# Kernel tuning notes

Hardware: AMD Instinct MI355X
Metric: run time of the kernel (lower is better)

Reference implementation:

```python
import jax, jax.numpy as jnp
import numpy as np
from jax import lax

D_MODEL = 1024
D_INNER = 2048   # expand * d_model
D_STATE = 16
DT_RANK = 64     # ceil(d_model / 16)
D_CONV = 4
B, L = 2, 1024


def setup_inputs() -> dict:
    key = jax.random.key(0)
    ks = jax.random.split(key, 8)
    s = 0.02
    x = jax.random.normal(ks[0], (B, L, D_MODEL), dtype=jnp.float32)
    in_proj_w = jax.random.normal(ks[1], (2 * D_INNER, D_MODEL), dtype=jnp.float32) * s
    conv_w = jax.random.normal(ks[2], (D_INNER, D_CONV), dtype=jnp.float32) * s  # depthwise kernel
    conv_b = jax.random.normal(ks[3], (D_INNER,), dtype=jnp.float32) * s
    x_proj_w = jax.random.normal(ks[4], (DT_RANK + 2 * D_STATE, D_INNER), dtype=jnp.float32) * s
    dt_proj_w = jax.random.normal(ks[5], (D_INNER, DT_RANK), dtype=jnp.float32) * s
    dt_proj_b = jax.random.normal(ks[6], (D_INNER,), dtype=jnp.float32) * s
    A_log = jnp.log(jnp.broadcast_to(jnp.arange(1, D_STATE + 1, dtype=jnp.float32), (D_INNER, D_STATE)))
    D = jnp.ones((D_INNER,), dtype=jnp.float32)
    out_proj_w = jax.random.normal(ks[7], (D_MODEL, D_INNER), dtype=jnp.float32) * s
    return {"x": x, "in_proj_w": in_proj_w, "conv_w": conv_w, "conv_b": conv_b,
            "x_proj_w": x_proj_w, "dt_proj_w": dt_proj_w, "dt_proj_b": dt_proj_b,
            "A_log": A_log, "D": D, "out_proj_w": out_proj_w}


def _causal_depthwise_conv(x, conv_w, conv_b):
    # x: (B, L, d_inner); torch Conv1d(padding=d_conv-1) then [:, :, :L] == causal left pad
    Lx = x.shape[1]
    k = conv_w.shape[-1]
    xp = jnp.pad(x, ((0, 0), (k - 1, 0), (0, 0)))
    out = conv_b
    # small fixed kernel width (4): unrolled taps, fully vectorized over B,L,D
    out = sum(xp[:, i:i + Lx, :] * conv_w[:, i] for i in range(k)) + conv_b
    return out


def mamba_forward(x, in_proj_w, conv_w, conv_b, x_proj_w, dt_proj_w, dt_proj_b, A_log, D, out_proj_w):
    xz = x @ in_proj_w.T                       # (B, L, 2*d_inner)
    xi, z = xz[..., :D_INNER], xz[..., D_INNER:]
    xc = jax.nn.silu(_causal_depthwise_conv(xi, conv_w, conv_b))  # (B, L, d_inner)

    x_dbl = xc @ x_proj_w.T                    # (B, L, dt_rank + 2*d_state)
    dt = x_dbl[..., :DT_RANK]
    Bm = x_dbl[..., DT_RANK:DT_RANK + D_STATE]  # (B, L, N)
    Cm = x_dbl[..., DT_RANK + D_STATE:]         # (B, L, N)
    delta = jax.nn.softplus(dt @ dt_proj_w.T + dt_proj_b)  # (B, L, d_inner)

    A = -jnp.exp(A_log)                        # (d_inner, N)
    deltaA = jnp.exp(delta[..., None] * A)                           # (B, L, D, N)
    deltaBx = delta[..., None] * Bm[:, :, None, :] * xc[..., None]   # (B, L, D, N)

    def step(h, inp):
        dA, dBx, Ct = inp                      # (B,D,N), (B,D,N), (B,N)
        h = dA * h + dBx
        y = jnp.einsum('bdn,bn->bd', h, Ct)
        return h, y

    h0 = jnp.zeros((x.shape[0], D_INNER, D_STATE), dtype=x.dtype)
    _, ys = lax.scan(step, h0, (deltaA.transpose(1, 0, 2, 3),
                                deltaBx.transpose(1, 0, 2, 3),
                                Cm.transpose(1, 0, 2)))
    y = ys.transpose(1, 0, 2)                  # (B, L, d_inner)
    y = y + xc * D
    y = y * jax.nn.silu(z)
    return y @ out_proj_w.T                    # (B, L, d_model)


def reference(x, in_proj_w, conv_w, conv_b, x_proj_w, dt_proj_w, dt_proj_b, A_log, D, out_proj_w):
    return mamba_forward(x, in_proj_w, conv_w, conv_b, x_proj_w, dt_proj_w, dt_proj_b, A_log, D, out_proj_w)
```

## Files before the change

kernel.cpp:

```cpp
#include <hip/hip_runtime.h>
#include <hip/hip_bf16.h>
#include <cstdint>
#include <cstddef>

#define DMODEL 1024
#define DINNER 2048
#define NSTATE 16
#define DTRANK 64
#define BATCH 2
#define SEQ 1024
#define ROWS (BATCH*SEQ)
#define NCHUNK 16
#define CLEN (SEQ/NCHUNK)
#define KSPLIT 16

typedef __attribute__((ext_vector_type(8))) short short8;
typedef __attribute__((ext_vector_type(4))) float f32x4;

__device__ __forceinline__ float bf2f(__hip_bfloat16 h){ return __bfloat162float(h); }
__device__ __forceinline__ float sigmoidf_(float x){ return 1.0f/(1.0f + __expf(-x)); }

__device__ __forceinline__ void gld16(const void* g, void* l){
  __builtin_amdgcn_global_load_lds((const __attribute__((address_space(1))) void*)g,
                                   (__attribute__((address_space(3))) void*)l, 16, 0, 0);
}

__global__ void sniff_k(const unsigned short* __restrict__ xu, int* __restrict__ flag)
{
  int t = threadIdx.x;
  int cnt = 0;
  for (int i = t; i < 1024; i += 64) {
    unsigned short u = xu[i];
    int e = (u >> 7) & 0xFF;
    if (e >= 0x70 && e <= 0x86) cnt++;
  }
  for (int o = 32; o; o >>= 1) cnt += __shfl_down(cnt, o);
  if (t == 0) *flag = (cnt >= 768) ? 0 : 1;
}

struct CvtArgs {
  const void *s0,*s1,*s2,*s3,*s4,*s5,*s6,*s7,*s8,*s9;
  __hip_bfloat16 *xB,*inpB,*xprojB,*dtprojB,*outpB;
  float *cwF,*cbF,*dtbF,*alF,*DF;
  float *outZ;
  const int* flag;
};
#define CVT_C1 2097152
#define CVT_C2 6291456
#define CVT_C3 6299648
#define CVT_C4 6301696
#define CVT_C5 6498304
#define CVT_C6 6629376
#define CVT_C7 6631424
#define CVT_C8 6664192
#define CVT_C9 6666240
#define CVT_TOT 8763392

__device__ __forceinline__ float cvt_read(const void* s, int j, int fl){
  return fl ? ((const float*)s)[j] : bf2f(((const __hip_bfloat16*)s)[j]);
}

__global__ __launch_bounds__(256)
void convert_all_k(CvtArgs a)
{
  int i = blockIdx.x * 256 + threadIdx.x;
  const int fl = *a.flag;

  if (blockIdx.x < 2048) {
    f32x4 z = {0.f, 0.f, 0.f, 0.f};
    ((f32x4*)a.outZ)[i] = z;
  }

  if (i >= CVT_TOT) return;
  if (i < CVT_C1)      a.xB[i]                = __float2bfloat16(cvt_read(a.s0, i, fl));
  else if (i < CVT_C2) a.inpB[i-CVT_C1]       = __float2bfloat16(cvt_read(a.s1, i-CVT_C1, fl));
  else if (i < CVT_C3) a.cwF[i-CVT_C2]        = cvt_read(a.s2, i-CVT_C2, fl);
  else if (i < CVT_C4) a.cbF[i-CVT_C3]        = cvt_read(a.s3, i-CVT_C3, fl);
  else if (i < CVT_C5) a.xprojB[i-CVT_C4]     = __float2bfloat16(cvt_read(a.s4, i-CVT_C4, fl));
  else if (i < CVT_C6) a.dtprojB[i-CVT_C5]    = __float2bfloat16(cvt_read(a.s5, i-CVT_C5, fl));
  else if (i < CVT_C7) a.dtbF[i-CVT_C6]       = cvt_read(a.s6, i-CVT_C6, fl);
  else if (i < CVT_C8) a.alF[i-CVT_C7]        = cvt_read(a.s7, i-CVT_C7, fl);
  else if (i < CVT_C9) a.DF[i-CVT_C8]         = cvt_read(a.s8, i-CVT_C8, fl);
  else                 a.outpB[i-CVT_C9]      = __float2bfloat16(cvt_read(a.s9, i-CVT_C9, fl));
}

template<int EPI>
__global__ __launch_bounds__(256)
void gemm64(const __hip_bfloat16* __restrict__ A,
            const __hip_bfloat16* __restrict__ W,
            int M, int N, int K, int kchunk,
            float* __restrict__ outF,
            __hip_bfloat16* __restrict__ outH,
            const float* __restrict__ biasF)
{
  __shared__ alignas(16) __hip_bfloat16 As[128*64];
  __shared__ alignas(16) __hip_bfloat16 Ws[128*64];
  const int tid  = threadIdx.x;
  const int lane = tid & 63;
  const int wave = tid >> 6;
  const int wm = wave & 1, wn = wave >> 1;
  const int row0 = blockIdx.y * 128;
  const int col0 = blockIdx.x * 128;

  f32x4 acc[4][4] = {};

  int kbeg = 0, kend = K;
  if (EPI == 5 || EPI == 6) { kbeg = blockIdx.z * kchunk; kend = kbeg + kchunk; }

  const int r16 = lane & 15, q = lane >> 4;
  const int sx0 = ((q ^ (r16 & 7)) * 16);

  for (int k0 = kbeg; k0 < kend; k0 += 64) {
#pragma unroll
    for (int j = 0; j < 4; ++j) {
      int e = tid + j*256;
      int r = e >> 3, g = e & 7;
      int kc = ((g ^ (r & 7)) << 3);
      gld16(A + (size_t)(row0 + r) * K + k0 + kc, (char*)As + (size_t)e*16);
    }
#pragma unroll
    for (int j = 0; j < 4; ++j) {
      int e = tid + j*256;
      int r = e >> 3, g = e & 7;
      int kc = ((g ^ (r & 7)) << 3);
      int rw = col0 + r; if (EPI == 5 && rw > N-1) rw = N-1;
      gld16(W + (size_t)rw * K + k0 + kc, (char*)Ws + (size_t)e*16);
    }
    __syncthreads();

    const char* Ab = (const char*)As + ((wm*64 + r16) * 128);
    const char* Wb = (const char*)Ws + ((wn*64 + r16) * 128);
#pragma unroll
    for (int ksub = 0; ksub < 2; ++ksub) {
      const int sx = sx0 ^ (ksub * 64);
      short8 af[4], wf[4];
#pragma unroll
      for (int i = 0; i < 4; ++i) af[i] = *(const short8*)(Ab + i*16*128 + sx);
#pragma unroll
      for (int i = 0; i < 4; ++i) wf[i] = *(const short8*)(Wb + i*16*128 + sx);
#pragma unroll
      for (int mt = 0; mt < 4; ++mt)
#pragma unroll
        for (int nt = 0; nt < 4; ++nt)
          acc[mt][nt] = __builtin_amdgcn_mfma_f32_16x16x32_bf16(af[mt], wf[nt], acc[mt][nt], 0, 0, 0);
    }
    __syncthreads();
  }

  const int mbase = row0 + wm*64 + (q * 4);
  const int nbase = col0 + wn*64 + r16;

  float bv[4];
  if (EPI == 3) {
#pragma unroll
    for (int nt = 0; nt < 4; ++nt) bv[nt] = biasF[nbase + nt*16];
  }

#pragma unroll
  for (int mt = 0; mt < 4; ++mt) {
#pragma unroll
    for (int nt = 0; nt < 4; ++nt) {
#pragma unroll
      for (int r = 0; r < 4; ++r) {
        int row = mbase + mt*16 + r;
        int col = nbase + nt*16;
        float v = acc[mt][nt][r];
        if (EPI == 3) {
          v += bv[nt];
          float sp = fmaxf(v, 0.0f) + __logf(1.0f + __expf(-fabsf(v)));
          outF[(size_t)row * DINNER + col] = sp;
        } else if (EPI == 4) {
          if (col < DINNER) {
            outH[(size_t)row * DINNER + col] = __float2bfloat16(v);
          } else {
            outF[(size_t)row * DINNER + (col - DINNER)] = v * sigmoidf_(v);
          }
        } else if (EPI == 5) {
          if (col < 96)
            outF[(size_t)blockIdx.z * (ROWS*96) + (size_t)row * 96 + col] = v;
        } else if (EPI == 6) {
          unsafeAtomicAdd(&outF[(size_t)row * DMODEL + col], v);
        }
      }
    }
  }
}

__global__ __launch_bounds__(256)
void reduce_xdbl_k(const float* __restrict__ part, float* __restrict__ xdbl,
                   __hip_bfloat16* __restrict__ dtH)
{
  int i = blockIdx.x * 256 + threadIdx.x;
  if (i >= ROWS*96) return;
  float s = 0.f;
#pragma unroll
  for (int kc = 0; kc < KSPLIT; ++kc) s += part[(size_t)kc*ROWS*96 + i];
  xdbl[i] = s;
  int row = i / 96, col = i - row*96;
  if (col < 64) dtH[(size_t)row*64 + col] = __float2bfloat16(s);
}

__global__ __launch_bounds__(256)
void conv_silu_k(const __hip_bfloat16* __restrict__ xi,
                 const float* __restrict__ cw,
                 const float* __restrict__ cb,
                 __hip_bfloat16* __restrict__ xcH)
{
  int idx = blockIdx.x * 256 + threadIdx.x;
  if (idx >= ROWS * DINNER) return;
  int d  = idx & (DINNER - 1);
  int t  = (idx >> 11) & (SEQ - 1);
  int bt = idx >> 11;
  float acc = cb[d];
#pragma unroll
  for (int i = 0; i < 4; ++i) {
    int tt = t - 3 + i;
    if (tt >= 0) acc += cw[d*4 + i] * bf2f(xi[(size_t)(bt - 3 + i) * DINNER + d]);
  }
  float y = acc * sigmoidf_(acc);
  xcH[idx] = __float2bfloat16(y);
}

#define GSTEP 8

__global__ __launch_bounds__(256)
void stats_k(const float* __restrict__ delta,
             const __hip_bfloat16* __restrict__ xcH,
             const float* __restrict__ xdbl,
             const float* __restrict__ alF,
             float* __restrict__ Hc, float* __restrict__ Sd)
{
  __shared__ alignas(16) float Bs[CLEN*16];
  const int bid  = blockIdx.x;
  const int b    = bid >> 9;
  const int c    = (bid >> 5) & (NCHUNK-1);
  const int cg   = bid & 31;
  const int tid  = threadIdx.x;
  const int lane = tid & 63;
  const int wave = tid >> 6;
  const int sub  = lane & 3;
  const int ch   = (cg << 6) + (wave << 4) + (lane >> 2);

  const size_t rb = (size_t)b * SEQ + (size_t)c * CLEN;

  for (int i = tid; i < CLEN*16; i += 256) {
    int t = i >> 4, j = i & 15;
    Bs[i] = xdbl[(rb + t)*96 + 64 + j];
  }
  __syncthreads();

  float negA[4];
#pragma unroll
  for (int j = 0; j < 4; ++j) negA[j] = -__expf(alF[ch*NSTATE + sub*4 + j]);

  const float*          dp = delta + rb * DINNER + ch;
  const __hip_bfloat16* xp = xcH   + rb * DINNER + ch;

  float h0=0.f,h1=0.f,h2=0.f,h3=0.f, sd=0.f;
  float d0[GSTEP], x0[GSTEP], d1[GSTEP], x1[GSTEP];

#define PF1(D_,X_,T0) \
  _Pragma("unroll") \
  for (int u = 0; u < GSTEP; ++u) { \
    D_[u] = dp[(size_t)((T0)+u) * DINNER]; \
    X_[u] = bf2f(xp[(size_t)((T0)+u) * DINNER]); \
  }
#define ST1(D_,X_,T0) \
  _Pragma("unroll") \
  for (int u = 0; u < GSTEP; ++u) { \
    float d_ = D_[u]; \
    sd += d_; \
    float du = d_ * X_[u]; \
    f32x4 B4 = *(const f32x4*)&Bs[((T0)+u)*16 + sub*4]; \
    h0 = __expf(d_*negA[0])*h0 + du*B4.x; \
    h1 = __expf(d_*negA[1])*h1 + du*B4.y; \
    h2 = __expf(d_*negA[2])*h2 + du*B4.z; \
    h3 = __expf(d_*negA[3])*h3 + du*B4.w; \
  }

  PF1(d0, x0, 0)
  for (int t0 = 0; t0 < CLEN; t0 += 2*GSTEP) {
    PF1(d1, x1, t0 + GSTEP)
    ST1(d0, x0, t0)
    if (t0 + 2*GSTEP < CLEN) { PF1(d0, x0, t0 + 2*GSTEP) }
    ST1(d1, x1, t0 + GSTEP)
  }
#undef PF1
#undef ST1

  const size_t bc = (size_t)(b*NCHUNK + c);
  f32x4 hv = { h0, h1, h2, h3 };
  *(f32x4*)&Hc[(bc*DINNER + ch)*NSTATE + sub*4] = hv;
  if (sub == 0) Sd[bc*DINNER + ch] = sd;
}

__global__ __launch_bounds__(256)
void carry_k(const float* __restrict__ Hc, const float* __restrict__ Sd,
             const float* __restrict__ alF, float* __restrict__ hin)
{
  int i = blockIdx.x * 256 + threadIdx.x;
  int n  = i & (NSTATE-1);
  int ch = (i >> 4) & (DINNER-1);
  int b  = i >> 15;
  float negA = -__expf(alF[ch * NSTATE + n]);
  float h = 0.f;
#pragma unroll
  for (int c = 0; c < NCHUNK; ++c) {
    size_t bc = (size_t)(b*NCHUNK + c);
    hin[(bc*DINNER + ch)*NSTATE + n] = h;
    float P = __expf(negA * Sd[bc*DINNER + ch]);
    h = P * h + Hc[(bc*DINNER + ch)*NSTATE + n];
  }
}

__global__ __launch_bounds__(256)
void emit_k(const float* __restrict__ delta,
            const __hip_bfloat16* __restrict__ xcH,
            const float* __restrict__ xdbl,
            const float* __restrict__ zsF,
            const float* __restrict__ alF,
            const float* __restrict__ DF,
            const float* __restrict__ hin,
            __hip_bfloat16* __restrict__ yH)
{
  __shared__ alignas(16) float BCs[CLEN*32];
  const int bid  = blockIdx.x;
  const int b    = bid >> 9;
  const int c    = (bid >> 5) & (NCHUNK-1);
  const int cg   = bid & 31;
  const int tid  = threadIdx.x;
  const int lane = tid & 63;
  const int wave = tid >> 6;
  const int sub  = lane & 3;
  const int ch   = (cg << 6) + (wave << 4) + (lane >> 2);

  const size_t rb = (size_t)b * SEQ + (size_t)c * CLEN;

  for (int i = tid; i < CLEN*32; i += 256) {
    int t = i >> 5, j = i & 31;
    BCs[i] = xdbl[(rb + t)*96 + 64 + j];
  }
  __syncthreads();

  float negA[4];
#pragma unroll
  for (int j = 0; j < 4; ++j) negA[j] = -__expf(alF[ch*NSTATE + sub*4 + j]);
  const float Dch = DF[ch];

  const float*          dp = delta + rb * DINNER + ch;
  const __hip_bfloat16* xp = xcH   + rb * DINNER + ch;
  const float*          zp = zsF   + rb * DINNER + ch;
  __hip_bfloat16*       yp = yH    + rb * DINNER + ch;

  f32x4 hv = *(const f32x4*)&hin[((size_t)(b*NCHUNK + c)*DINNER + ch)*NSTATE + sub*4];
  float h0=hv.x, h1=hv.y, h2=hv.z, h3=hv.w;

  float d0[GSTEP], x0[GSTEP], z0[GSTEP], d1[GSTEP], x1[GSTEP], z1[GSTEP];

#define PF(D_,X_,Z_,T0) \
  _Pragma("unroll") \
  for (int u = 0; u < GSTEP; ++u) { \
    D_[u] = dp[(size_t)((T0)+u) * DINNER]; \
    X_[u] = bf2f(xp[(size_t)((T0)+u) * DINNER]); \
    Z_[u] = zp[(size_t)((T0)+u) * DINNER]; \
  }
#define STEPS(D_,X_,Z_,T0) \
  _Pragma("unroll") \
  for (int u = 0; u < GSTEP; ++u) { \
    float d_ = D_[u]; \
    float du = d_ * X_[u]; \
    f32x4 B4 = *(const f32x4*)&BCs[((T0)+u)*32 + sub*4]; \
    f32x4 C4 = *(const f32x4*)&BCs[((T0)+u)*32 + 16 + sub*4]; \
    h0 = __expf(d_*negA[0])*h0 + du*B4.x; \
    h1 = __expf(d_*negA[1])*h1 + du*B4.y; \
    h2 = __expf(d_*negA[2])*h2 + du*B4.z; \
    h3 = __expf(d_*negA[3])*h3 + du*B4.w; \
    float p = h0*C4.x + h1*C4.y + h2*C4.z + h3*C4.w; \
    p += __shfl_xor(p, 1); \
    p += __shfl_xor(p, 2); \
    if (sub == 0) { \
      float y = (p + X_[u] * Dch) * Z_[u]; \
      yp[(size_t)((T0)+u) * DINNER] = __float2bfloat16(y); \
    } \
  }

  PF(d0, x0, z0, 0)
  for (int t0 = 0; t0 < CLEN; t0 += 2*GSTEP) {
    PF(d1, x1, z1, t0 + GSTEP)
    STEPS(d0, x0, z0, t0)
    if (t0 + 2*GSTEP < CLEN) { PF(d0, x0, z0, t0 + 2*GSTEP) }
    STEPS(d1, x1, z1, t0 + GSTEP)
  }
#undef PF
#undef STEPS
}

extern "C" void kernel_launch(void* const* d_in, const int* in_sizes, int n_in,
                              void* d_out, int out_size, void* d_ws, size_t ws_size,
                              hipStream_t stream)
{
  float* out = (float*)d_out;
  char* ws = (char*)d_ws;
  const size_t MB = 1024*1024;

  int*            flag    = (int*)            (ws);
  float*          cwF     = (float*)          (ws + 1024);
  float*          cbF     = (float*)          (ws + 40*1024);
  float*          dtbF    = (float*)          (ws + 56*1024);
  float*          alF     = (float*)          (ws + 72*1024);
  float*          DF      = (float*)          (ws + 208*1024);
  float*          Sd      = (float*)          (ws + 256*1024);
  __hip_bfloat16* xB      = (__hip_bfloat16*) (ws + 1*MB);
  __hip_bfloat16* inpB    = (__hip_bfloat16*) (ws + 5*MB);
  __hip_bfloat16* xiB     = (__hip_bfloat16*) (ws + 13*MB);
  float*          part    = (float*)          (ws + 1*MB);
  float*          dlt     = (float*)          (ws + 1*MB);
  __hip_bfloat16* xprojB  = (__hip_bfloat16*) (ws + 21*MB);
  __hip_bfloat16* dtprojB = (__hip_bfloat16*) (ws + 21*MB + 512*1024);
  __hip_bfloat16* outpB   = (__hip_bfloat16*) (ws + 22*MB);
  float*          zsF     = (float*)          (ws + 26*MB);
  __hip_bfloat16* xcH     = (__hip_bfloat16*) (ws + 42*MB);
  float*          xdbl    = (float*)          (ws + 50*MB);
  __hip_bfloat16* dtH     = (__hip_bfloat16*) (ws + 51*MB);
  __hip_bfloat16* yH      = (__hip_bfloat16*) (ws + 52*MB);
  float*          Hc      = (float*)          (ws + 60*MB);
  float*          hin     = (float*)          (ws + 64*MB);

  dim3 blk(256);

  sniff_k<<<1, 64, 0, stream>>>((const unsigned short*)d_in[0], flag);
  CvtArgs ca = { d_in[0], d_in[1], d_in[2], d_in[3], d_in[4],
                 d_in[5], d_in[6], d_in[7], d_in[8], d_in[9],
                 xB, inpB, xprojB, dtprojB, outpB,
                 cwF, cbF, dtbF, alF, DF, out, flag };
  convert_all_k<<<CVT_TOT/256, blk, 0, stream>>>(ca);

  gemm64<4><<<dim3(4096/128, ROWS/128), blk, 0, stream>>>(
      xB, inpB, ROWS, 2*DINNER, DMODEL, 0, zsF, xiB, nullptr);

  conv_silu_k<<<(ROWS*DINNER)/256, blk, 0, stream>>>(xiB, cwF, cbF, xcH);

  gemm64<5><<<dim3(1, ROWS/128, KSPLIT), blk, 0, stream>>>(
      xcH, xprojB, ROWS, 96, DINNER, DINNER/KSPLIT, part, nullptr, nullptr);
  reduce_xdbl_k<<<(ROWS*96+255)/256, blk, 0, stream>>>(part, xdbl, dtH);

  gemm64<3><<<dim3(DINNER/128, ROWS/128), blk, 0, stream>>>(
      dtH, dtprojB, ROWS, DINNER, DTRANK, 0, dlt, nullptr, dtbF);

  stats_k<<<BATCH*NCHUNK*32, blk, 0, stream>>>(dlt, xcH, xdbl, alF, Hc, Sd);
  carry_k<<<(BATCH*DINNER*NSTATE)/256, blk, 0, stream>>>(Hc, Sd, alF, hin);
  emit_k<<<BATCH*NCHUNK*32, blk, 0, stream>>>(dlt, xcH, xdbl, zsF, alF, DF, hin, yH);

  gemm64<6><<<dim3(DMODEL/128, ROWS/128, 4), blk, 0, stream>>>(
      yH, outpB, ROWS, DMODEL, DINNER, DINNER/4, out, nullptr, nullptr);
}
```

Baseline: 264.2 us.

## Vectorize input conversion, store gate in bf16, deepen scan prefetch

```diff
diff --git a/kernel.cpp b/kernel.cpp
--- a/kernel.cpp
+++ b/kernel.cpp
@@ -15,10 +15,19 @@
 #define KSPLIT 16
 
 typedef __attribute__((ext_vector_type(8))) short short8;
+typedef __attribute__((ext_vector_type(4))) short short4v;
 typedef __attribute__((ext_vector_type(4))) float f32x4;
 
 __device__ __forceinline__ float bf2f(__hip_bfloat16 h){ return __bfloat162float(h); }
 __device__ __forceinline__ float sigmoidf_(float x){ return 1.0f/(1.0f + __expf(-x)); }
+__device__ __forceinline__ unsigned short f2bfbits(float v){
+  __hip_bfloat16 h = __float2bfloat16(v);
+  return *(unsigned short*)&h;
+}
+__device__ __forceinline__ float bfbits2f(unsigned short u){
+  unsigned int x = ((unsigned int)u) << 16;
+  return *(float*)&x;
+}
 
 __device__ __forceinline__ void gld16(const void* g, void* l){
   __builtin_amdgcn_global_load_lds((const __attribute__((address_space(1))) void*)g,
@@ -55,33 +64,53 @@
 #define CVT_C8 6664192
 #define CVT_C9 6666240
 #define CVT_TOT 8763392
-
-__device__ __forceinline__ float cvt_read(const void* s, int j, int fl){
-  return fl ? ((const float*)s)[j] : bf2f(((const __hip_bfloat16*)s)[j]);
+#define CVT_BLOCKS (CVT_TOT/4/256)
+
+__device__ __forceinline__ void cvt_read4(const void* s, int j, int fl, float v[4]){
+  if (fl) {
+    f32x4 t = ((const f32x4*)s)[j>>2];
+    v[0]=t.x; v[1]=t.y; v[2]=t.z; v[3]=t.w;
+  } else {
+    short4v t = *(const short4v*)((const __hip_bfloat16*)s + j);
+    v[0]=bfbits2f((unsigned short)t.x); v[1]=bfbits2f((unsigned short)t.y);
+    v[2]=bfbits2f((unsigned short)t.z); v[3]=bfbits2f((unsigned short)t.w);
+  }
+}
+__device__ __forceinline__ void cvt_wB(__hip_bfloat16* d, int j, const float v[4]){
+  short4v o;
+  o.x=(short)f2bfbits(v[0]); o.y=(short)f2bfbits(v[1]);
+  o.z=(short)f2bfbits(v[2]); o.w=(short)f2bfbits(v[3]);
+  *(short4v*)(d + j) = o;
+}
+__device__ __forceinline__ void cvt_wF(float* d, int j, const float v[4]){
+  f32x4 o = { v[0], v[1], v[2], v[3] };
+  *(f32x4*)(d + j) = o;
 }
 
 __global__ __launch_bounds__(256)
 void convert_all_k(CvtArgs a)
 {
-  int i = blockIdx.x * 256 + threadIdx.x;
+  int i4 = blockIdx.x * 256 + threadIdx.x;
   const int fl = *a.flag;
 
   if (blockIdx.x < 2048) {
     f32x4 z = {0.f, 0.f, 0.f, 0.f};
-    ((f32x4*)a.outZ)[i] = z;
-  }
-
+    ((f32x4*)a.outZ)[i4] = z;
+  }
+
+  int i = i4 * 4;
   if (i >= CVT_TOT) return;
-  if (i < CVT_C1)      a.xB[i]                = __float2bfloat16(cvt_read(a.s0, i, fl));
-  else if (i < CVT_C2) a.inpB[i-CVT_C1]       = __float2bfloat16(cvt_read(a.s1, i-CVT_C1, fl));
-  else if (i < CVT_C3) a.cwF[i-CVT_C2]        = cvt_read(a.s2, i-CVT_C2, fl);
-  else if (i < CVT_C4) a.cbF[i-CVT_C3]        = cvt_read(a.s3, i-CVT_C3, fl);
-  else if (i < CVT_C5) a.xprojB[i-CVT_C4]     = __float2bfloat16(cvt_read(a.s4, i-CVT_C4, fl));
-  else if (i < CVT_C6) a.dtprojB[i-CVT_C5]    = __float2bfloat16(cvt_read(a.s5, i-CVT_C5, fl));
-  else if (i < CVT_C7) a.dtbF[i-CVT_C6]       = cvt_read(a.s6, i-CVT_C6, fl);
-  else if (i < CVT_C8) a.alF[i-CVT_C7]        = cvt_read(a.s7, i-CVT_C7, fl);
-  else if (i < CVT_C9) a.DF[i-CVT_C8]         = cvt_read(a.s8, i-CVT_C8, fl);
-  else                 a.outpB[i-CVT_C9]      = __float2bfloat16(cvt_read(a.s9, i-CVT_C9, fl));
+  float v[4];
+  if (i < CVT_C1)      { cvt_read4(a.s0, i, fl, v);        cvt_wB(a.xB, i, v); }
+  else if (i < CVT_C2) { cvt_read4(a.s1, i-CVT_C1, fl, v); cvt_wB(a.inpB, i-CVT_C1, v); }
+  else if (i < CVT_C3) { cvt_read4(a.s2, i-CVT_C2, fl, v); cvt_wF(a.cwF, i-CVT_C2, v); }
+  else if (i < CVT_C4) { cvt_read4(a.s3, i-CVT_C3, fl, v); cvt_wF(a.cbF, i-CVT_C3, v); }
+  else if (i < CVT_C5) { cvt_read4(a.s4, i-CVT_C4, fl, v); cvt_wB(a.xprojB, i-CVT_C4, v); }
+  else if (i < CVT_C6) { cvt_read4(a.s5, i-CVT_C5, fl, v); cvt_wB(a.dtprojB, i-CVT_C5, v); }
+  else if (i < CVT_C7) { cvt_read4(a.s6, i-CVT_C6, fl, v); cvt_wF(a.dtbF, i-CVT_C6, v); }
+  else if (i < CVT_C8) { cvt_read4(a.s7, i-CVT_C7, fl, v); cvt_wF(a.alF, i-CVT_C7, v); }
+  else if (i < CVT_C9) { cvt_read4(a.s8, i-CVT_C8, fl, v); cvt_wF(a.DF, i-CVT_C8, v); }
+  else                 { cvt_read4(a.s9, i-CVT_C9, fl, v); cvt_wB(a.outpB, i-CVT_C9, v); }
 }
 
 template<int EPI>
@@ -91,6 +120,7 @@
             int M, int N, int K, int kchunk,
             float* __restrict__ outF,
             __hip_bfloat16* __restrict__ outH,
+            __hip_bfloat16* __restrict__ outH2,
             const float* __restrict__ biasF)
 {
   __shared__ alignas(16) __hip_bfloat16 As[128*64];
@@ -173,7 +203,7 @@
           if (col < DINNER) {
             outH[(size_t)row * DINNER + col] = __float2bfloat16(v);
           } else {
-            outF[(size_t)row * DINNER + (col - DINNER)] = v * sigmoidf_(v);
+            outH2[(size_t)row * DINNER + (col - DINNER)] = __float2bfloat16(v * sigmoidf_(v));
           }
         } else if (EPI == 5) {
           if (col < 96)
@@ -221,7 +251,7 @@
   xcH[idx] = __float2bfloat16(y);
 }
 
-#define GSTEP 8
+#define GSTEP 16
 
 __global__ __launch_bounds__(256)
 void stats_k(const float* __restrict__ delta,
@@ -317,7 +347,7 @@
 void emit_k(const float* __restrict__ delta,
             const __hip_bfloat16* __restrict__ xcH,
             const float* __restrict__ xdbl,
-            const float* __restrict__ zsF,
+            const __hip_bfloat16* __restrict__ zsH,
             const float* __restrict__ alF,
             const float* __restrict__ DF,
             const float* __restrict__ hin,
@@ -349,7 +379,7 @@
 
   const float*          dp = delta + rb * DINNER + ch;
   const __hip_bfloat16* xp = xcH   + rb * DINNER + ch;
-  const float*          zp = zsF   + rb * DINNER + ch;
+  const __hip_bfloat16* zp = zsH   + rb * DINNER + ch;
   __hip_bfloat16*       yp = yH    + rb * DINNER + ch;
 
   f32x4 hv = *(const f32x4*)&hin[((size_t)(b*NCHUNK + c)*DINNER + ch)*NSTATE + sub*4];
@@ -362,7 +392,7 @@
   for (int u = 0; u < GSTEP; ++u) { \
     D_[u] = dp[(size_t)((T0)+u) * DINNER]; \
     X_[u] = bf2f(xp[(size_t)((T0)+u) * DINNER]); \
-    Z_[u] = zp[(size_t)((T0)+u) * DINNER]; \
+    Z_[u] = bf2f(zp[(size_t)((T0)+u) * DINNER]); \
   }
 #define STEPS(D_,X_,Z_,T0) \
   _Pragma("unroll") \
@@ -418,7 +448,7 @@
   __hip_bfloat16* xprojB  = (__hip_bfloat16*) (ws + 21*MB);
   __hip_bfloat16* dtprojB = (__hip_bfloat16*) (ws + 21*MB + 512*1024);
   __hip_bfloat16* outpB   = (__hip_bfloat16*) (ws + 22*MB);
-  float*          zsF     = (float*)          (ws + 26*MB);
+  __hip_bfloat16* zsH     = (__hip_bfloat16*) (ws + 26*MB);
   __hip_bfloat16* xcH     = (__hip_bfloat16*) (ws + 42*MB);
   float*          xdbl    = (float*)          (ws + 50*MB);
   __hip_bfloat16* dtH     = (__hip_bfloat16*) (ws + 51*MB);
@@ -433,24 +463,24 @@
                  d_in[5], d_in[6], d_in[7], d_in[8], d_in[9],
                  xB, inpB, xprojB, dtprojB, outpB,
                  cwF, cbF, dtbF, alF, DF, out, flag };
-  convert_all_k<<<CVT_TOT/256, blk, 0, stream>>>(ca);
+  convert_all_k<<<CVT_BLOCKS, blk, 0, stream>>>(ca);
 
   gemm64<4><<<dim3(4096/128, ROWS/128), blk, 0, stream>>>(
-      xB, inpB, ROWS, 2*DINNER, DMODEL, 0, zsF, xiB, nullptr);
+      xB, inpB, ROWS, 2*DINNER, DMODEL, 0, nullptr, xiB, zsH, nullptr);
 
   conv_silu_k<<<(ROWS*DINNER)/256, blk, 0, stream>>>(xiB, cwF, cbF, xcH);
 
   gemm64<5><<<dim3(1, ROWS/128, KSPLIT), blk, 0, stream>>>(
-      xcH, xprojB, ROWS, 96, DINNER, DINNER/KSPLIT, part, nullptr, nullptr);
+      xcH, xprojB, ROWS, 96, DINNER, DINNER/KSPLIT, part, nullptr, nullptr, nullptr);
   reduce_xdbl_k<<<(ROWS*96+255)/256, blk, 0, stream>>>(part, xdbl, dtH);
 
   gemm64<3><<<dim3(DINNER/128, ROWS/128), blk, 0, stream>>>(
-      dtH, dtprojB, ROWS, DINNER, DTRANK, 0, dlt, nullptr, dtbF);
+      dtH, dtprojB, ROWS, DINNER, DTRANK, 0, dlt, nullptr, nullptr, dtbF);
 
   stats_k<<<BATCH*NCHUNK*32, blk, 0, stream>>>(dlt, xcH, xdbl, alF, Hc, Sd);
   carry_k<<<(BATCH*DINNER*NSTATE)/256, blk, 0, stream>>>(Hc, Sd, alF, hin);
-  emit_k<<<BATCH*NCHUNK*32, blk, 0, stream>>>(dlt, xcH, xdbl, zsF, alF, DF, hin, yH);
+  emit_k<<<BATCH*NCHUNK*32, blk, 0, stream>>>(dlt, xcH, xdbl, zsH, alF, DF, hin, yH);
 
   gemm64<6><<<dim3(DMODEL/128, ROWS/128, 4), blk, 0, stream>>>(
-      yH, outpB, ROWS, DMODEL, DINNER, DINNER/4, out, nullptr, nullptr);
-}
+      yH, outpB, ROWS, DMODEL, DINNER, DINNER/4, out, nullptr, nullptr, nullptr);
+}
```

Result: slower. 275.7 us (+4.3%).
